# Kernel optimization log

Hardware: AMD Instinct MI355X
Metric: run time of the kernel (lower is better)

## Reference

```python
import jax, jax.numpy as jnp
import numpy as np

B, C_FEAT, C_COND, C_KEY, H, W = 4, 256, 256, 32, 64, 64


def setup_inputs() -> dict:
    key = jax.random.key(0)
    ks = jax.random.split(key, 8)
    s = 0.02
    return {
        "features": jax.random.normal(ks[0], (B, C_FEAT, H, W), jnp.float32),
        "conditions": jax.random.normal(ks[1], (B, C_COND, H, W), jnp.float32),
        "Wq": jax.random.normal(ks[2], (C_KEY, C_COND), jnp.float32) * s,
        "bq": jnp.zeros((C_KEY,), jnp.float32),
        "Wk": jax.random.normal(ks[3], (C_KEY, C_FEAT), jnp.float32) * s,
        "bk": jnp.zeros((C_KEY,), jnp.float32),
        "Wv": jax.random.normal(ks[4], (C_FEAT, C_FEAT), jnp.float32) * s,
        "bv": jnp.zeros((C_FEAT,), jnp.float32),
        "gamma": jnp.zeros((1,), jnp.float32),
    }


def reference(features, conditions, Wq, bq, Wk, bk, Wv, bv, gamma):
    b, c, h, w = features.shape
    n = h * w
    feat = features.reshape(b, c, n)            # [B, C, N]
    cond = conditions.reshape(b, cond_c := conditions.shape[1], n)
    # 1x1 convs == per-pixel linear projections
    q = jnp.einsum('kc,bcn->bnk', Wq, cond) + bq          # [B, N, Ck]
    k = jnp.einsum('kc,bcn->bkn', Wk, feat) + bk[:, None]  # [B, Ck, N]
    v = jnp.einsum('oc,bcn->bon', Wv, feat) + bv[:, None]  # [B, C, N]
    energy = jnp.einsum('bik,bkj->bij', q, k)             # [B, N, N]
    attn = jax.nn.softmax(energy, axis=-1)
    out = jnp.einsum('bcj,bij->bci', v, attn)             # [B, C, N]
    out = out.reshape(b, c, h, w)
    return gamma * out + features
```

## Files before the change

### kernel.cpp

```cpp
#include <hip/hip_runtime.h>

typedef __bf16 bf16_t;
typedef __bf16 bf16x4 __attribute__((ext_vector_type(4)));
typedef __bf16 bf16x8 __attribute__((ext_vector_type(8)));
typedef float f32x4 __attribute__((ext_vector_type(4)));

#define N_PIX 4096
#define CFEAT 256
#define CKEY 32
#define NBATCH 4

static __device__ __forceinline__ f32x4 mfma16(bf16x8 a, bf16x8 b, f32x4 c) {
    return __builtin_amdgcn_mfma_f32_16x16x32_bf16(a, b, c, 0, 0, 0);
}

static __device__ __forceinline__ void glds16(const void* g, void* l) {
    __builtin_amdgcn_global_load_lds(
        (const __attribute__((address_space(1))) void*)g,
        (__attribute__((address_space(3))) void*)l, 16, 0, 0);
}

__global__ __launch_bounds__(256) void projqk_kernel(
    const float* __restrict__ Wq, const float* __restrict__ bq, const float* __restrict__ Xq,
    const float* __restrict__ Wk, const float* __restrict__ bk, const float* __restrict__ Xk,
    bf16_t* __restrict__ Qt, bf16_t* __restrict__ Kt)
{
    __shared__ __attribute__((aligned(16))) bf16_t T[64][40];
    const int lane = threadIdx.x & 63, wave = threadIdx.x >> 6;
    const int g = lane >> 4, ln = lane & 15;
    const bool isK = (blockIdx.y == 1);
    const float* W    = isK ? Wk : Wq;
    const float* bias = isK ? bk : bq;
    const float* X  = (isK ? Xk : Xq) + (size_t)blockIdx.z * CFEAT * N_PIX;
    bf16_t*      Yt = (isK ? Kt : Qt) + (size_t)blockIdx.z * N_PIX * CKEY;

    const int m_base = (wave & 1) * 16;
    const int n_loc  = (wave >> 1) * 32;
    const int n_base = blockIdx.x * 64 + n_loc;

    f32x4 zero = {0.f, 0.f, 0.f, 0.f};
    f32x4 acc[2] = {zero, zero};
    for (int k0 = 0; k0 < CFEAT; k0 += 32) {
        bf16x8 a;
        const float* wp = W + (size_t)(m_base + ln) * CFEAT + k0 + g * 8;
#pragma unroll
        for (int j = 0; j < 8; ++j) a[j] = (bf16_t)wp[j];
#pragma unroll
        for (int nt = 0; nt < 2; ++nt) {
            const float* xp = X + (size_t)(k0 + g * 8) * N_PIX + n_base + nt * 16 + ln;
            bf16x8 bfr;
#pragma unroll
            for (int j = 0; j < 8; ++j) bfr[j] = (bf16_t)xp[(size_t)j * N_PIX];
            acc[nt] = mfma16(a, bfr, acc[nt]);
        }
    }
#pragma unroll
    for (int nt = 0; nt < 2; ++nt)
#pragma unroll
        for (int r = 0; r < 4; ++r) {
            const int ck = m_base + g * 4 + r;
            T[n_loc + nt * 16 + ln][ck] = (bf16_t)(acc[nt][r] + bias[ck]);
        }
    __syncthreads();
    const int n  = threadIdx.x >> 2;
    const int sg = threadIdx.x & 3;
    bf16x8 row = *(const bf16x8*)&T[n][sg * 8];
    *(bf16x8*)&Yt[(size_t)(blockIdx.x * 64 + n) * CKEY + sg * 8] = row;
}

__global__ __launch_bounds__(256, 4) void projv_kernel(
    const float* __restrict__ W, const float* __restrict__ bias,
    const float* __restrict__ X, bf16_t* __restrict__ V)
{
    const int lane = threadIdx.x & 63, wave = threadIdx.x >> 6;
    const int g = lane >> 4, ln = lane & 15;
    const int b = blockIdx.z;
    const int n_base = blockIdx.x * 32;
    const int c_wave = blockIdx.y * 128 + wave * 32;
    const float* Xb = X + (size_t)b * CFEAT * N_PIX;
    bf16_t*      Vb = V + (size_t)b * CFEAT * N_PIX;

    f32x4 zero = {0.f, 0.f, 0.f, 0.f};
    f32x4 acc[2][2];
#pragma unroll
    for (int mt = 0; mt < 2; ++mt) { acc[mt][0] = zero; acc[mt][1] = zero; }

    for (int k0 = 0; k0 < CFEAT; k0 += 32) {
        bf16x8 bfr[2];
#pragma unroll
        for (int nt = 0; nt < 2; ++nt) {
            const float* xp = Xb + (size_t)(k0 + g * 8) * N_PIX + n_base + nt * 16 + ln;
#pragma unroll
            for (int j = 0; j < 8; ++j) bfr[nt][j] = (bf16_t)xp[(size_t)j * N_PIX];
        }
#pragma unroll
        for (int mt = 0; mt < 2; ++mt) {
            const float* wp = W + (size_t)(c_wave + mt * 16 + ln) * CFEAT + k0 + g * 8;
            bf16x8 a;
#pragma unroll
            for (int j = 0; j < 8; ++j) a[j] = (bf16_t)wp[j];
            acc[mt][0] = mfma16(a, bfr[0], acc[mt][0]);
            acc[mt][1] = mfma16(a, bfr[1], acc[mt][1]);
        }
    }
#pragma unroll
    for (int mt = 0; mt < 2; ++mt)
#pragma unroll
        for (int nt = 0; nt < 2; ++nt)
#pragma unroll
            for (int r = 0; r < 4; ++r) {
                const int m = c_wave + mt * 16 + g * 4 + r;
                const int n = n_base + nt * 16 + ln;
                Vb[(size_t)m * N_PIX + n] = (bf16_t)(acc[mt][nt][r] + bias[m]);
            }
}

#define PSTRIDE 72
__global__ __launch_bounds__(256, 4) void pv_kernel(
    const bf16_t* __restrict__ Qt, const bf16_t* __restrict__ Kt,
    const bf16_t* __restrict__ V,
    const float* __restrict__ features, const float* __restrict__ gamma,
    float* __restrict__ out)
{
    __shared__ __attribute__((aligned(16))) bf16_t Vlds[3][64 * 64];
    __shared__ __attribute__((aligned(16))) bf16_t Plds[4][16 * PSTRIDE];

    const int lane = threadIdx.x & 63, wave = threadIdx.x >> 6;
    const int g = lane >> 4, ln = lane & 15;
    const int b = blockIdx.z;
    const int i_base = blockIdx.y * 64 + wave * 16;
    const int c_base = blockIdx.x * 64;

    const bf16_t* Qb = Qt + (size_t)b * N_PIX * CKEY;
    const bf16_t* Kb = Kt + (size_t)b * N_PIX * CKEY;
    const bf16_t* Vb = V + (size_t)b * CFEAT * N_PIX;
    bf16_t* Pw = &Plds[wave][0];

    const int s0 = wave * 128 + lane;
    const int s1 = s0 + 64;
    const int sc0 = s0 >> 3, sj0 = (s0 & 7) ^ (sc0 & 7);
    const int sc1 = s1 >> 3, sj1 = (s1 & 7) ^ (sc1 & 7);
    const bf16_t* vg0 = Vb + (size_t)(c_base + sc0) * N_PIX + sj0 * 8;
    const bf16_t* vg1 = Vb + (size_t)(c_base + sc1) * N_PIX + sj1 * 8;

    const bf16x8 qf = *(const bf16x8*)&Qb[(size_t)(i_base + ln) * CKEY + g * 8];

    f32x4 zero = {0.f, 0.f, 0.f, 0.f};
    f32x4 acc[4] = {zero, zero, zero, zero};
    float lsum = 0.f;

    glds16(vg0, &Vlds[0][(size_t)(wave * 128) * 8 ]);
    glds16(vg1, &Vlds[0][(size_t)(wave * 128 + 64) * 8 ]);

    int bcur = 0, bnxt = 1;
    for (int n = 0; n < 64; ++n) {
        const int j0 = n * 64;
        const int jn = (j0 + 64) & (N_PIX - 1);
        glds16(vg0 + jn, &Vlds[bnxt][(size_t)(wave * 128) * 8 ]);
        glds16(vg1 + jn, &Vlds[bnxt][(size_t)(wave * 128 + 64) * 8 ]);

        f32x4 st[4];
#pragma unroll
        for (int jt = 0; jt < 4; ++jt) {
            const bf16x8 kf = *(const bf16x8*)&Kb[(size_t)(j0 + jt * 16 + ln) * CKEY + g * 8];
            st[jt] = mfma16(kf, qf, zero);
        }
#pragma unroll
        for (int jt = 0; jt < 4; ++jt) {
            bf16x4 p;
#pragma unroll
            for (int r = 0; r < 4; ++r) { float e = __expf(st[jt][r]); lsum += e; p[r] = (bf16_t)e; }
            *(bf16x4*)&Pw[ln * PSTRIDE + jt * 16 + g * 4] = p;
        }
        const bf16x8 pa0 = *(const bf16x8*)&Pw[ln * PSTRIDE + g * 8];
        const bf16x8 pa1 = *(const bf16x8*)&Pw[ln * PSTRIDE + 32 + g * 8];

        __syncthreads();

        const bf16_t* Vt = &Vlds[bcur][0];
#pragma unroll
        for (int ct = 0; ct < 4; ++ct) {
            const int c = ct * 16 + ln;
            const int sl0 = c * 8 + ((g)     ^ (c & 7));
            const int sl1 = c * 8 + ((4 + g) ^ (c & 7));
            const bf16x8 v0 = *(const bf16x8*)&Vt[sl0 * 8];
            const bf16x8 v1 = *(const bf16x8*)&Vt[sl1 * 8];
            acc[ct] = mfma16(v0, pa0, acc[ct]);
            acc[ct] = mfma16(v1, pa1, acc[ct]);
        }
        const int bold = bcur;
        bcur = bnxt;
        bnxt = (bnxt == 2) ? 0 : (bnxt + 1);
        (void)bold;
    }

    lsum += __shfl_xor(lsum, 16);
    lsum += __shfl_xor(lsum, 32);
    const float s_lane = gamma[0] / lsum;

#pragma unroll
    for (int ct = 0; ct < 4; ++ct)
#pragma unroll
        for (int r = 0; r < 4; ++r) {
            const int c = c_base + ct * 16 + g * 4 + r;
            const int i = i_base + ln;
            const size_t idx = ((size_t)b * CFEAT + c) * N_PIX + i;
            out[idx] = s_lane * acc[ct][r] + features[idx];
        }
}

extern "C" void kernel_launch(void* const* d_in, const int* in_sizes, int n_in,
                              void* d_out, int out_size, void* d_ws, size_t ws_size,
                              hipStream_t stream) {
    const float* features   = (const float*)d_in[0];
    const float* conditions = (const float*)d_in[1];
    const float* Wq  = (const float*)d_in[2];
    const float* bq  = (const float*)d_in[3];
    const float* Wk  = (const float*)d_in[4];
    const float* bk  = (const float*)d_in[5];
    const float* Wv  = (const float*)d_in[6];
    const float* bv  = (const float*)d_in[7];
    const float* gam = (const float*)d_in[8];
    float* out = (float*)d_out;

    bf16_t* Qt = (bf16_t*)d_ws;
    bf16_t* Kt = Qt + (size_t)NBATCH * N_PIX * CKEY;
    bf16_t* Vw = Kt + (size_t)NBATCH * N_PIX * CKEY;

    projqk_kernel<<<dim3(N_PIX / 64, 2, NBATCH), 256, 0, stream>>>(
        Wq, bq, conditions, Wk, bk, features, Qt, Kt);
    projv_kernel<<<dim3(N_PIX / 32, 2, NBATCH), 256, 0, stream>>>(Wv, bv, features, Vw);
    pv_kernel<<<dim3(4, N_PIX / 64, NBATCH), 256, 0, stream>>>(
        Qt, Kt, Vw, features, gam, out);
}
```

Baseline: 197.8 us.

## Software-pipeline softmax with PV, transpose P in registers, fold log2e into Q

Restructures the attention loop so the exp/softmax tile for the next key block is computed while the current V tile is consumed by MFMAs. V staging grows to a 4-deep LDS ring with explicit vmcnt waits and a raw barrier. The P-tile LDS round-trip is replaced by packed bf16 plus permlane swaps. exp is switched to native exp2, with log2e folded into the Q projection. The row sum is split into four accumulators. This adds register pressure and relies on hand-written waitcnt and barrier ordering being correct.

```diff
diff --git a/kernel.cpp b/kernel.cpp
--- a/kernel.cpp
+++ b/kernel.cpp
@@ -1,15 +1,24 @@
 #include <hip/hip_runtime.h>
 
 typedef __bf16 bf16_t;
+typedef __bf16 bf16x2 __attribute__((ext_vector_type(2)));
 typedef __bf16 bf16x4 __attribute__((ext_vector_type(4)));
 typedef __bf16 bf16x8 __attribute__((ext_vector_type(8)));
 typedef float f32x4 __attribute__((ext_vector_type(4)));
+typedef unsigned u32;
+typedef unsigned u32x4 __attribute__((ext_vector_type(4)));
 
 #define N_PIX 4096
 #define CFEAT 256
 #define CKEY 32
 #define NBATCH 4
 
+#if __has_builtin(__builtin_amdgcn_exp2f)
+#define EXP2(x) __builtin_amdgcn_exp2f(x)
+#else
+#define EXP2(x) exp2f(x)
+#endif
+
 static __device__ __forceinline__ f32x4 mfma16(bf16x8 a, bf16x8 b, f32x4 c) {
     return __builtin_amdgcn_mfma_f32_16x16x32_bf16(a, b, c, 0, 0, 0);
 }
@@ -18,6 +27,60 @@
     __builtin_amdgcn_global_load_lds(
         (const __attribute__((address_space(1))) void*)g,
         (__attribute__((address_space(3))) void*)l, 16, 0, 0);
+}
+
+static __device__ __forceinline__ u32 pk2(float lo, float hi) {
+    bf16x2 t; t[0] = (bf16_t)lo; t[1] = (bf16_t)hi;
+    return __builtin_bit_cast(u32, t);
+}
+
+static __device__ __forceinline__ void xpose4(u32 &x, u32 &y) {
+#if __has_builtin(__builtin_amdgcn_permlane32_swap) && __has_builtin(__builtin_amdgcn_permlane16_swap)
+    auto r32 = __builtin_amdgcn_permlane32_swap(x, y, false, false);
+    auto r16 = __builtin_amdgcn_permlane16_swap(r32[0], r32[1], false, false);
+    x = r16[0]; y = r16[1];
+#else
+    const int lane = threadIdx.x & 63;
+    const int g = lane >> 4, ln = lane & 15;
+    const int i0 = ln + ((g & 1) << 5);
+    const int i2 = i0 + 16;
+    u32 xs0 = (u32)__shfl((int)x, i0), ys0 = (u32)__shfl((int)y, i0);
+    u32 xs2 = (u32)__shfl((int)x, i2), ys2 = (u32)__shfl((int)y, i2);
+    x = (g < 2) ? xs0 : ys0;
+    y = (g < 2) ? xs2 : ys2;
+#endif
+}
+
+static __device__ __forceinline__ void softmax_tile(
+    const bf16x8 kf[4], bf16x8 qf, bool addl,
+    float &ls0, float &ls1, float &ls2, float &ls3,
+    bf16x8 &pa0, bf16x8 &pa1)
+{
+    f32x4 zero = {0.f, 0.f, 0.f, 0.f};
+    f32x4 st[4];
+#pragma unroll
+    for (int jt = 0; jt < 4; ++jt) st[jt] = mfma16(kf[jt], qf, zero);
+    float ex[16];
+#pragma unroll
+    for (int jt = 0; jt < 4; ++jt)
+#pragma unroll
+        for (int r = 0; r < 4; ++r) ex[jt * 4 + r] = EXP2(st[jt][r]);
+    if (addl) {
+#pragma unroll
+        for (int t = 0; t < 16; t += 4) {
+            ls0 += ex[t]; ls1 += ex[t + 1]; ls2 += ex[t + 2]; ls3 += ex[t + 3];
+        }
+    }
+    u32 a0 = pk2(ex[0],  ex[1]),  a1 = pk2(ex[2],  ex[3]);
+    u32 b0 = pk2(ex[4],  ex[5]),  b1 = pk2(ex[6],  ex[7]);
+    u32 c0 = pk2(ex[8],  ex[9]),  c1 = pk2(ex[10], ex[11]);
+    u32 d0 = pk2(ex[12], ex[13]), d1 = pk2(ex[14], ex[15]);
+    xpose4(a0, b0); xpose4(a1, b1);
+    xpose4(c0, d0); xpose4(c1, d1);
+    u32x4 w0 = {a0, a1, b0, b1};
+    u32x4 w1 = {c0, c1, d0, d1};
+    pa0 = __builtin_bit_cast(bf16x8, w0);
+    pa1 = __builtin_bit_cast(bf16x8, w1);
 }
 
 __global__ __launch_bounds__(256) void projqk_kernel(
@@ -33,6 +96,7 @@
     const float* bias = isK ? bk : bq;
     const float* X  = (isK ? Xk : Xq) + (size_t)blockIdx.z * CFEAT * N_PIX;
     bf16_t*      Yt = (isK ? Kt : Qt) + (size_t)blockIdx.z * N_PIX * CKEY;
+    const float qscale = isK ? 1.0f : 1.4426950408889634f;
 
     const int m_base = (wave & 1) * 16;
     const int n_loc  = (wave >> 1) * 32;
@@ -59,7 +123,7 @@
 #pragma unroll
         for (int r = 0; r < 4; ++r) {
             const int ck = m_base + g * 4 + r;
-            T[n_loc + nt * 16 + ln][ck] = (bf16_t)(acc[nt][r] + bias[ck]);
+            T[n_loc + nt * 16 + ln][ck] = (bf16_t)((acc[nt][r] + bias[ck]) * qscale);
         }
     __syncthreads();
     const int n  = threadIdx.x >> 2;
@@ -115,15 +179,13 @@
             }
 }
 
-#define PSTRIDE 72
 __global__ __launch_bounds__(256, 4) void pv_kernel(
     const bf16_t* __restrict__ Qt, const bf16_t* __restrict__ Kt,
     const bf16_t* __restrict__ V,
     const float* __restrict__ features, const float* __restrict__ gamma,
     float* __restrict__ out)
 {
-    __shared__ __attribute__((aligned(16))) bf16_t Vlds[3][64 * 64];
-    __shared__ __attribute__((aligned(16))) bf16_t Plds[4][16 * PSTRIDE];
+    __shared__ __attribute__((aligned(16))) bf16_t Vlds[4][64 * 64];
 
     const int lane = threadIdx.x & 63, wave = threadIdx.x >> 6;
     const int g = lane >> 4, ln = lane & 15;
@@ -134,7 +196,6 @@
     const bf16_t* Qb = Qt + (size_t)b * N_PIX * CKEY;
     const bf16_t* Kb = Kt + (size_t)b * N_PIX * CKEY;
     const bf16_t* Vb = V + (size_t)b * CFEAT * N_PIX;
-    bf16_t* Pw = &Plds[wave][0];
 
     const int s0 = wave * 128 + lane;
     const int s1 = s0 + 64;
@@ -147,53 +208,63 @@
 
     f32x4 zero = {0.f, 0.f, 0.f, 0.f};
     f32x4 acc[4] = {zero, zero, zero, zero};
-    float lsum = 0.f;
-
-    glds16(vg0, &Vlds[0][(size_t)(wave * 128) * 8 ]);
-    glds16(vg1, &Vlds[0][(size_t)(wave * 128 + 64) * 8 ]);
-
-    int bcur = 0, bnxt = 1;
+    float ls0 = 0.f, ls1 = 0.f, ls2 = 0.f, ls3 = 0.f;
+
+    bf16x8 pa0c, pa1c;
+    {
+        bf16x8 kf[4];
+#pragma unroll
+        for (int jt = 0; jt < 4; ++jt)
+            kf[jt] = *(const bf16x8*)&Kb[(size_t)(jt * 16 + ln) * CKEY + g * 8];
+        asm volatile("" ::: "memory");
+        glds16(vg0,      &Vlds[0][wave * 1024]);
+        glds16(vg1,      &Vlds[0][wave * 1024 + 512]);
+        glds16(vg0 + 64, &Vlds[1][wave * 1024]);
+        glds16(vg1 + 64, &Vlds[1][wave * 1024 + 512]);
+        softmax_tile(kf, qf, true, ls0, ls1, ls2, ls3, pa0c, pa1c);
+        asm volatile("s_waitcnt vmcnt(2)" ::: "memory");
+        __builtin_amdgcn_s_barrier();
+        asm volatile("" ::: "memory");
+    }
+
     for (int n = 0; n < 64; ++n) {
-        const int j0 = n * 64;
-        const int jn = (j0 + 64) & (N_PIX - 1);
-        glds16(vg0 + jn, &Vlds[bnxt][(size_t)(wave * 128) * 8 ]);
-        glds16(vg1 + jn, &Vlds[bnxt][(size_t)(wave * 128 + 64) * 8 ]);
-
-        f32x4 st[4];
-#pragma unroll
-        for (int jt = 0; jt < 4; ++jt) {
-            const bf16x8 kf = *(const bf16x8*)&Kb[(size_t)(j0 + jt * 16 + ln) * CKEY + g * 8];
-            st[jt] = mfma16(kf, qf, zero);
-        }
-#pragma unroll
-        for (int jt = 0; jt < 4; ++jt) {
-            bf16x4 p;
-#pragma unroll
-            for (int r = 0; r < 4; ++r) { float e = __expf(st[jt][r]); lsum += e; p[r] = (bf16_t)e; }
-            *(bf16x4*)&Pw[ln * PSTRIDE + jt * 16 + g * 4] = p;
-        }
-        const bf16x8 pa0 = *(const bf16x8*)&Pw[ln * PSTRIDE + g * 8];
-        const bf16x8 pa1 = *(const bf16x8*)&Pw[ln * PSTRIDE + 32 + g * 8];
-
-        __syncthreads();
-
-        const bf16_t* Vt = &Vlds[bcur][0];
+        const bf16_t* Vt = &Vlds[n & 3][0];
+        bf16x8 vf[8];
 #pragma unroll
         for (int ct = 0; ct < 4; ++ct) {
             const int c = ct * 16 + ln;
-            const int sl0 = c * 8 + ((g)     ^ (c & 7));
-            const int sl1 = c * 8 + ((4 + g) ^ (c & 7));
-            const bf16x8 v0 = *(const bf16x8*)&Vt[sl0 * 8];
-            const bf16x8 v1 = *(const bf16x8*)&Vt[sl1 * 8];
-            acc[ct] = mfma16(v0, pa0, acc[ct]);
-            acc[ct] = mfma16(v1, pa1, acc[ct]);
-        }
-        const int bold = bcur;
-        bcur = bnxt;
-        bnxt = (bnxt == 2) ? 0 : (bnxt + 1);
-        (void)bold;
-    }
-
+            vf[2 * ct]     = *(const bf16x8*)&Vt[(c * 8 + ( g      ^ (c & 7))) * 8];
+            vf[2 * ct + 1] = *(const bf16x8*)&Vt[(c * 8 + ((4 + g) ^ (c & 7))) * 8];
+        }
+
+        const int jq = ((n + 1) & 63) * 64;
+        bf16x8 kf[4];
+#pragma unroll
+        for (int jt = 0; jt < 4; ++jt)
+            kf[jt] = *(const bf16x8*)&Kb[(size_t)(jq + jt * 16 + ln) * CKEY + g * 8];
+        asm volatile("" ::: "memory");
+
+        const int jn = (n * 64 + 128) & (N_PIX - 1);
+        bf16_t* ldst = &Vlds[(n + 2) & 3][wave * 1024];
+        glds16(vg0 + jn, ldst);
+        glds16(vg1 + jn, ldst + 512);
+
+        bf16x8 pa0n, pa1n;
+        softmax_tile(kf, qf, n < 63, ls0, ls1, ls2, ls3, pa0n, pa1n);
+
+        asm volatile("s_waitcnt vmcnt(2)" ::: "memory");
+        __builtin_amdgcn_s_barrier();
+        asm volatile("" ::: "memory");
+
+#pragma unroll
+        for (int ct = 0; ct < 4; ++ct) {
+            acc[ct] = mfma16(vf[2 * ct],     pa0c, acc[ct]);
+            acc[ct] = mfma16(vf[2 * ct + 1], pa1c, acc[ct]);
+        }
+        pa0c = pa0n; pa1c = pa1n;
+    }
+
+    float lsum = (ls0 + ls1) + (ls2 + ls3);
     lsum += __shfl_xor(lsum, 16);
     lsum += __shfl_xor(lsum, 32);
     const float s_lane = gamma[0] / lsum;
```

Result: faster. 193.0 us (-2.4%).
